# Performance work log

Hardware: AMD Instinct MI355X
Metric: run time of the kernel (lower is better)

## Reference

```python
import jax, jax.numpy as jnp
import numpy as np

N, C, K, H = 131072, 512, 128, 8  # points, channels, patch_size, heads


def setup_inputs() -> dict:
    key = jax.random.key(0)
    ks = jax.random.split(key, 6)
    feat = jax.random.normal(ks[0], (N, C), dtype=jnp.float32)
    Wqkv = jax.random.normal(ks[1], (C, 3 * C), dtype=jnp.float32) * 0.02
    bqkv = jax.random.normal(ks[2], (3 * C,), dtype=jnp.float32) * 0.02
    Wproj = jax.random.normal(ks[3], (C, C), dtype=jnp.float32) * 0.02
    bproj = jax.random.normal(ks[4], (C,), dtype=jnp.float32) * 0.02
    order = jax.random.permutation(ks[5], N).astype(jnp.int64)  # serialized order (all clusters full)
    inverse = jnp.argsort(order).astype(jnp.int64)              # serialized inverse
    return {"feat": feat, "Wqkv": Wqkv, "bqkv": bqkv, "Wproj": Wproj,
            "bproj": bproj, "order": order, "inverse": inverse}


def reference(feat, Wqkv, bqkv, Wproj, bproj, order, inverse):
    hd = C // H
    scale = hd ** -0.5
    qkv = feat @ Wqkv + bqkv                 # [N, 3C]
    qkv = qkv[order]                         # gather by serialized order
    qkv = qkv.reshape(-1, K, 3, H, hd)       # [W, K, 3, H, hd]
    qkv = jnp.moveaxis(qkv, 2, 0)            # [3, W, K, H, hd]
    q = jnp.swapaxes(qkv[0], 1, 2)           # [W, H, K, hd]
    k = jnp.swapaxes(qkv[1], 1, 2)
    v = jnp.swapaxes(qkv[2], 1, 2)
    # upcast_attention / upcast_softmax -> compute scores & softmax in fp32
    attn = jnp.einsum('whkd,whjd->whkj', (q * scale).astype(jnp.float32),
                      k.astype(jnp.float32))             # [W, H, K, K]
    attn = jax.nn.softmax(attn, axis=-1).astype(feat.dtype)
    out = jnp.einsum('whkj,whjd->whkd', attn, v)          # [W, H, K, hd]
    out = jnp.swapaxes(out, 1, 2).reshape(-1, C)          # [N, C]
    out = out[inverse]                                    # scatter back via inverse
    out = out @ Wproj + bproj
    return out
```

## Files before the change

### kernel.cpp

```cpp
#include <hip/hip_runtime.h>
#include <hip/hip_bf16.h>
#include <cstdint>
#include <cstddef>

typedef __bf16 bf16;
typedef __bf16 bf16x8 __attribute__((ext_vector_type(8)));
typedef float f32x4 __attribute__((ext_vector_type(4)));

#define N_PTS 131072
#define CDIM  512
#define C3    1536
#define HD    64
#define NH    8
#define KWIN  128

static __device__ __forceinline__ bf16 cvt(float x) { return (bf16)x; }

static __device__ __forceinline__ void gld16(const bf16* g, bf16* l) {
    __builtin_amdgcn_global_load_lds(
        (const __attribute__((address_space(1))) void*)g,
        (__attribute__((address_space(3))) void*)l, 16, 0, 0);
}

__global__ __launch_bounds__(256) void k_prep(
    const float* __restrict__ Wqkv, const float* __restrict__ Wproj,
    bf16* __restrict__ Wqkv_t, bf16* __restrict__ Wproj_t)
{
    int idx = blockIdx.x * 256 + threadIdx.x;
    if (idx < CDIM * C3) {
        int k = idx / C3, c = idx % C3;
        Wqkv_t[(size_t)c * CDIM + k] = cvt(Wqkv[idx]);
    } else {
        int j = idx - CDIM * C3;
        if (j < CDIM * CDIM) {
            int k = j / CDIM, c = j % CDIM;
            Wproj_t[(size_t)c * CDIM + k] = cvt(Wproj[j]);
        }
    }
}

__global__ __launch_bounds__(256) void k_gather(
    const float* __restrict__ feat, const int* __restrict__ order,
    bf16* __restrict__ feat_g)
{
    int row = blockIdx.x * 2 + (threadIdx.x >> 7);
    int c   = (threadIdx.x & 127) << 2;
    int src = order[row];
    float4 v = *reinterpret_cast<const float4*>(feat + (size_t)src * CDIM + c);
    union { bf16 e[4]; uint2 u; } pk;
    pk.e[0] = cvt(v.x); pk.e[1] = cvt(v.y); pk.e[2] = cvt(v.z); pk.e[3] = cvt(v.w);
    *reinterpret_cast<uint2*>(feat_g + (size_t)row * CDIM + c) = pk.u;
}

template <bool F32OUT, int NT>
__global__ __launch_bounds__(512) void k_gemm8(
    const bf16* __restrict__ Ag, const bf16* __restrict__ Bt,
    const float* __restrict__ bias, void* __restrict__ outp)
{
    __shared__ __align__(16) bf16 As[2][256 * 64];
    __shared__ __align__(16) bf16 Bs[2][256 * 64];

    const int t    = threadIdx.x;
    const int lane = t & 63;
    const int wv   = t >> 6;
    const int wr   = wv >> 2;
    const int wc   = wv & 3;
    const int g    = lane >> 4, r16 = lane & 15;

    const int nwg = gridDim.x;
    const int bid = blockIdx.x;
    const int swz = (bid & 7) * (nwg >> 3) + (bid >> 3);
    const int m0  = (swz / NT) * 256;
    const int n0  = (swz % NT) * 256;

    const int NKT = CDIM / 64;

    int aSrc[2][2], bSrc[2][2];
    int dstE[2][2];
#pragma unroll
    for (int h = 0; h < 2; ++h)
#pragma unroll
        for (int j = 0; j < 2; ++j) {
            int L = wv * 128 + j * 64 + lane;
            int row_l = L >> 3, p8 = L & 7;
            int s8 = (p8 - (row_l & 7)) & 7;
            int grow = h * 128 + row_l;
            aSrc[h][j] = (m0 + grow) * CDIM + s8 * 8;
            bSrc[h][j] = (n0 + grow) * CDIM + s8 * 8;
            dstE[h][j] = h * 8192 + (wv * 128 + j * 64) * 8;
        }

    int aoff[2][2][4];
    int boff[2][4];
#pragma unroll
    for (int grp = 0; grp < 2; ++grp)
#pragma unroll
        for (int kh = 0; kh < 2; ++kh)
#pragma unroll
            for (int q = 0; q < 4; ++q) {
                int row = wr * 128 + (grp * 4 + q) * 16 + r16;
                aoff[grp][kh][q] = row * 128 +
                    (((kh * 4 + g + (r16 & 7)) & 7) << 4);
            }
#pragma unroll
    for (int kh = 0; kh < 2; ++kh)
#pragma unroll
        for (int n = 0; n < 4; ++n) {
            int row = wc * 64 + n * 16 + r16;
            boff[kh][n] = row * 128 +
                (((kh * 4 + g + (r16 & 7)) & 7) << 4);
        }

    f32x4 acc[8][4];
    const f32x4 z = {0.f, 0.f, 0.f, 0.f};
#pragma unroll
    for (int i = 0; i < 8; ++i)
#pragma unroll
        for (int n = 0; n < 4; ++n) acc[i][n] = z;

    bf16x8 afr[2][4], bfr[2][4];

    auto stageA = [&](int tau) {
        const int b = tau & 1, ko = tau * 64;
#pragma unroll
        for (int h = 0; h < 2; ++h)
#pragma unroll
            for (int j = 0; j < 2; ++j)
                gld16(Ag + aSrc[h][j] + ko, &As[b][dstE[h][j]]);
    };
    auto stageB = [&](int tau) {
        const int b = tau & 1, ko = tau * 64;
#pragma unroll
        for (int h = 0; h < 2; ++h)
#pragma unroll
            for (int j = 0; j < 2; ++j)
                gld16(Bt + bSrc[h][j] + ko, &Bs[b][dstE[h][j]]);
    };
    auto readA = [&](int set, int b, int grp, int kh) {
        const char* ab = reinterpret_cast<const char*>(&As[b][0]);
#pragma unroll
        for (int q = 0; q < 4; ++q)
            afr[set][q] = *reinterpret_cast<const bf16x8*>(ab + aoff[grp][kh][q]);
    };
    auto readB = [&](int b, int kh) {
        const char* bb = reinterpret_cast<const char*>(&Bs[b][0]);
#pragma unroll
        for (int n = 0; n < 4; ++n)
            bfr[kh][n] = *reinterpret_cast<const bf16x8*>(bb + boff[kh][n]);
    };

    stageB(0); stageA(0); stageB(1); stageA(1);
    asm volatile("s_waitcnt vmcnt(8)" ::: "memory");
    __builtin_amdgcn_s_barrier();
    readA(0, 0, 0, 0);
    readB(0, 0);
    asm volatile("s_waitcnt lgkmcnt(0)" ::: "memory");
    __builtin_amdgcn_sched_barrier(0);

#pragma unroll
    for (int tau = 0; tau < NKT; ++tau) {
#pragma unroll
        for (int p = 0; p < 4; ++p) {
            const int pi  = tau * 4 + p;
            const int grp = p & 1, kh = p >> 1;

            if (p == 2 && tau + 2 < NKT) stageB(tau + 2);
            if (p == 3 && tau + 2 < NKT) stageA(tau + 2);

            if (pi + 1 < NKT * 4) {
                const int pn   = (p + 1) & 3;
                const int taun = tau + (p == 3);
                const int bn   = taun & 1;
                readA((pi + 1) & 1, bn, pn & 1, pn >> 1);
                if (pn == 0 || pn == 2) readB(bn, pn >> 1);
            }

            __builtin_amdgcn_s_setprio(1);
#pragma unroll
            for (int q = 0; q < 4; ++q)
#pragma unroll
                for (int n = 0; n < 4; ++n)
                    acc[grp * 4 + q][n] = __builtin_amdgcn_mfma_f32_16x16x32_bf16(
                        afr[pi & 1][q], bfr[kh][n], acc[grp * 4 + q][n], 0, 0, 0);
            __builtin_amdgcn_s_setprio(0);

            asm volatile("s_waitcnt lgkmcnt(0)" ::: "memory");
            __builtin_amdgcn_sched_barrier(0);
            if (p == 2) {
                if (tau + 2 < NKT)
                    asm volatile("s_waitcnt vmcnt(4)" ::: "memory");
                else
                    asm volatile("s_waitcnt vmcnt(0)" ::: "memory");
            }
            __builtin_amdgcn_s_barrier();
        }
    }

    const int ldo = NT * 256;
#pragma unroll
    for (int n = 0; n < 4; ++n) {
        int col = n0 + wc * 64 + n * 16 + r16;
        float b = bias[col];
#pragma unroll
        for (int i = 0; i < 8; ++i)
#pragma unroll
            for (int j = 0; j < 4; ++j) {
                int row = m0 + wr * 128 + i * 16 + g * 4 + j;
                if (F32OUT)
                    reinterpret_cast<float*>(outp)[(size_t)row * ldo + col] =
                        acc[i][n][j] + b;
                else
                    reinterpret_cast<bf16*>(outp)[(size_t)row * ldo + col] =
                        cvt(acc[i][n][j] + b);
            }
    }
}

__global__ __launch_bounds__(256) void k_attn(
    const bf16* __restrict__ qkv_s, const int* __restrict__ order,
    bf16* __restrict__ attn_g)
{
    __shared__ __align__(16) char smem[36864 + 64 * 136 * 2];
    __shared__ int ord_s[KWIN];
    bf16 (*Q)[72]   = reinterpret_cast<bf16 (*)[72]>(smem);
    bf16 (*Kt)[72]  = reinterpret_cast<bf16 (*)[72]>(smem + 128 * 72 * 2);
    bf16 (*P)[136]  = reinterpret_cast<bf16 (*)[136]>(smem);
    bf16 (*Vt)[136] = reinterpret_cast<bf16 (*)[136]>(smem + 36864);

    const int t    = threadIdx.x;
    const int lane = t & 63;
    const int wv   = t >> 6;
    const int g    = lane >> 4, r16 = lane & 15;
    const int h    = blockIdx.x;
    const int w    = blockIdx.y;

    const bf16* base = qkv_s + (size_t)w * KWIN * C3 + h * HD;

    if (t < KWIN) ord_s[t] = order[w * KWIN + t];

#pragma unroll
    for (int it = 0; it < 4; ++it) {
        int s   = it * 256 + t;
        int tok = s >> 3;
        int c8  = (s & 7) << 3;
        size_t roff = (size_t)tok * C3 + c8;
        *reinterpret_cast<uint4*>(&Q[tok][c8])  =
            *reinterpret_cast<const uint4*>(base + roff);
        *reinterpret_cast<uint4*>(&Kt[tok][c8]) =
            *reinterpret_cast<const uint4*>(base + roff + CDIM);
        uint4 vvec = *reinterpret_cast<const uint4*>(base + roff + 2 * CDIM);
        const bf16* ve = reinterpret_cast<const bf16*>(&vvec);
#pragma unroll
        for (int i = 0; i < 8; ++i) Vt[c8 + i][tok] = ve[i];
    }
    __syncthreads();

    f32x4 sc[2][8];
    const f32x4 z = {0.f, 0.f, 0.f, 0.f};
#pragma unroll
    for (int m = 0; m < 2; ++m)
#pragma unroll
        for (int n = 0; n < 8; ++n) sc[m][n] = z;

#pragma unroll
    for (int ks = 0; ks < 2; ++ks) {
        bf16x8 aq[2];
#pragma unroll
        for (int m = 0; m < 2; ++m)
            aq[m] = *reinterpret_cast<const bf16x8*>(
                &Q[wv * 32 + m * 16 + r16][ks * 32 + g * 8]);
#pragma unroll
        for (int n = 0; n < 8; ++n) {
            bf16x8 bk = *reinterpret_cast<const bf16x8*>(
                &Kt[n * 16 + r16][ks * 32 + g * 8]);
#pragma unroll
            for (int m = 0; m < 2; ++m)
                sc[m][n] = __builtin_amdgcn_mfma_f32_16x16x32_bf16(
                    aq[m], bk, sc[m][n], 0, 0, 0);
        }
    }

    const float scale = 0.125f;
    float inv_sum[2][4];
#pragma unroll
    for (int m = 0; m < 2; ++m) {
#pragma unroll
        for (int j = 0; j < 4; ++j) {
            float mx = -3.0e38f;
#pragma unroll
            for (int n = 0; n < 8; ++n) mx = fmaxf(mx, sc[m][n][j]);
            mx = fmaxf(mx, __shfl_xor(mx, 1));
            mx = fmaxf(mx, __shfl_xor(mx, 2));
            mx = fmaxf(mx, __shfl_xor(mx, 4));
            mx = fmaxf(mx, __shfl_xor(mx, 8));
            mx *= scale;
            float ssum = 0.f;
#pragma unroll
            for (int n = 0; n < 8; ++n) {
                float p = __expf(sc[m][n][j] * scale - mx);
                sc[m][n][j] = p;
                ssum += p;
            }
            ssum += __shfl_xor(ssum, 1);
            ssum += __shfl_xor(ssum, 2);
            ssum += __shfl_xor(ssum, 4);
            ssum += __shfl_xor(ssum, 8);
            inv_sum[m][j] = 1.f / ssum;
        }
    }

    __syncthreads();

#pragma unroll
    for (int m = 0; m < 2; ++m)
#pragma unroll
        for (int n = 0; n < 8; ++n)
#pragma unroll
            for (int j = 0; j < 4; ++j)
                P[wv * 32 + m * 16 + g * 4 + j][n * 16 + r16] =
                    cvt(sc[m][n][j] * inv_sum[m][j]);

    f32x4 o[2][4];
#pragma unroll
    for (int m = 0; m < 2; ++m)
#pragma unroll
        for (int n = 0; n < 4; ++n) o[m][n] = z;

#pragma unroll
    for (int kt = 0; kt < 4; ++kt) {
        bf16x8 ap[2];
#pragma unroll
        for (int m = 0; m < 2; ++m)
            ap[m] = *reinterpret_cast<const bf16x8*>(
                &P[wv * 32 + m * 16 + r16][kt * 32 + g * 8]);
#pragma unroll
        for (int n = 0; n < 4; ++n) {
            bf16x8 bvv = *reinterpret_cast<const bf16x8*>(
                &Vt[n * 16 + r16][kt * 32 + g * 8]);
#pragma unroll
            for (int m = 0; m < 2; ++m)
                o[m][n] = __builtin_amdgcn_mfma_f32_16x16x32_bf16(
                    ap[m], bvv, o[m][n], 0, 0, 0);
        }
    }

#pragma unroll
    for (int m = 0; m < 2; ++m)
#pragma unroll
        for (int n = 0; n < 4; ++n)
#pragma unroll
            for (int j = 0; j < 4; ++j) {
                int tok  = wv * 32 + m * 16 + g * 4 + j;
                int d    = n * 16 + r16;
                int drow = ord_s[tok];
                attn_g[(size_t)drow * CDIM + h * HD + d] = cvt(o[m][n][j]);
            }
}

extern "C" void kernel_launch(void* const* d_in, const int* in_sizes, int n_in,
                              void* d_out, int out_size, void* d_ws, size_t ws_size,
                              hipStream_t stream)
{
    const float* feat    = (const float*)d_in[0];
    const float* Wqkv    = (const float*)d_in[1];
    const float* bqkv    = (const float*)d_in[2];
    const float* Wproj   = (const float*)d_in[3];
    const float* bproj   = (const float*)d_in[4];
    const int*   order   = (const int*)d_in[5];
    float* out = (float*)d_out;

    const size_t qkv_bytes = (size_t)N_PTS * C3 * sizeof(bf16);
    const size_t gat_bytes = (size_t)N_PTS * CDIM * sizeof(bf16);
    const size_t wq_bytes  = (size_t)C3 * CDIM * sizeof(bf16);
    const size_t wp_bytes  = (size_t)CDIM * CDIM * sizeof(bf16);
    if (ws_size < qkv_bytes + gat_bytes + wq_bytes + wp_bytes) return;

    bf16* qkv_s     = (bf16*)d_ws;
    bf16* shared134 = (bf16*)((char*)d_ws + qkv_bytes);
    bf16* Wqkv_t    = (bf16*)((char*)d_ws + qkv_bytes + gat_bytes);
    bf16* Wproj_t   = (bf16*)((char*)d_ws + qkv_bytes + gat_bytes + wq_bytes);

    k_prep<<<dim3((CDIM * C3 + CDIM * CDIM + 255) / 256), 256, 0, stream>>>(
        Wqkv, Wproj, Wqkv_t, Wproj_t);
    k_gather<<<dim3(N_PTS / 2), 256, 0, stream>>>(feat, order, shared134);
    k_gemm8<false, C3 / 256><<<dim3((N_PTS / 256) * (C3 / 256)), 512, 0, stream>>>(
        shared134, Wqkv_t, bqkv, qkv_s);
    k_attn<<<dim3(NH, N_PTS / KWIN), 256, 0, stream>>>(qkv_s, order, shared134);
    k_gemm8<true, CDIM / 256><<<dim3((N_PTS / 256) * (CDIM / 256)), 512, 0, stream>>>(
        shared134, Wproj_t, bproj, out);
}
```

Measured before the change: 626.9 us.

## Fuse attention with output projection into per-window kernel

Merges the attention kernel and the output projection GEMM into one kernel, one block per window with 512 threads, looping over all 8 heads. Each head's attention output stays in LDS and is multiplied right away by the matching 64-column slice of Wproj. The results accumulate in registers and are scattered to the output via the order indices with bias added. This drops the bf16 attention intermediate round trip through HBM and one kernel launch. In exchange it uses about 138KB of LDS per block, which caps occupancy at one block per CU, and it serialises the heads with several barriers per head.

```diff
diff --git a/kernel.cpp b/kernel.cpp
--- a/kernel.cpp
+++ b/kernel.cpp
@@ -52,10 +52,10 @@
     *reinterpret_cast<uint2*>(feat_g + (size_t)row * CDIM + c) = pk.u;
 }
 
-template <bool F32OUT, int NT>
+template <int NT>
 __global__ __launch_bounds__(512) void k_gemm8(
     const bf16* __restrict__ Ag, const bf16* __restrict__ Bt,
-    const float* __restrict__ bias, void* __restrict__ outp)
+    const float* __restrict__ bias, bf16* __restrict__ outp)
 {
     __shared__ __align__(16) bf16 As[2][256 * 64];
     __shared__ __align__(16) bf16 Bs[2][256 * 64];
@@ -75,8 +75,7 @@
 
     const int NKT = CDIM / 64;
 
-    int aSrc[2][2], bSrc[2][2];
-    int dstE[2][2];
+    int aSrc[2][2], bSrc[2][2], dstE[2][2];
 #pragma unroll
     for (int h = 0; h < 2; ++h)
 #pragma unroll
@@ -206,89 +205,106 @@
 #pragma unroll
             for (int j = 0; j < 4; ++j) {
                 int row = m0 + wr * 128 + i * 16 + g * 4 + j;
-                if (F32OUT)
-                    reinterpret_cast<float*>(outp)[(size_t)row * ldo + col] =
-                        acc[i][n][j] + b;
-                else
-                    reinterpret_cast<bf16*>(outp)[(size_t)row * ldo + col] =
-                        cvt(acc[i][n][j] + b);
-            }
-    }
-}
-
-__global__ __launch_bounds__(256) void k_attn(
-    const bf16* __restrict__ qkv_s, const int* __restrict__ order,
-    bf16* __restrict__ attn_g)
+                outp[(size_t)row * ldo + col] = cvt(acc[i][n][j] + b);
+            }
+    }
+}
+
+__global__ __launch_bounds__(512) void k_attn_proj(
+    const bf16* __restrict__ qkv_s, const bf16* __restrict__ Wp_t,
+    const float* __restrict__ bproj, const int* __restrict__ order,
+    float* __restrict__ out)
 {
-    __shared__ __align__(16) char smem[36864 + 64 * 136 * 2];
+    __shared__ __align__(16) char smem[138240];
     __shared__ int ord_s[KWIN];
     bf16 (*Q)[72]   = reinterpret_cast<bf16 (*)[72]>(smem);
-    bf16 (*Kt)[72]  = reinterpret_cast<bf16 (*)[72]>(smem + 128 * 72 * 2);
+    bf16 (*Kt)[72]  = reinterpret_cast<bf16 (*)[72]>(smem + 18432);
     bf16 (*P)[136]  = reinterpret_cast<bf16 (*)[136]>(smem);
     bf16 (*Vt)[136] = reinterpret_cast<bf16 (*)[136]>(smem + 36864);
+    bf16 (*Oh)[72]  = reinterpret_cast<bf16 (*)[72]>(smem + 54272);
+    bf16* Wp        = reinterpret_cast<bf16*>(smem + 72704);
 
     const int t    = threadIdx.x;
     const int lane = t & 63;
     const int wv   = t >> 6;
     const int g    = lane >> 4, r16 = lane & 15;
-    const int h    = blockIdx.x;
-    const int w    = blockIdx.y;
-
-    const bf16* base = qkv_s + (size_t)w * KWIN * C3 + h * HD;
+    const int w    = blockIdx.x;
 
     if (t < KWIN) ord_s[t] = order[w * KWIN + t];
 
-#pragma unroll
-    for (int it = 0; it < 4; ++it) {
-        int s   = it * 256 + t;
-        int tok = s >> 3;
-        int c8  = (s & 7) << 3;
-        size_t roff = (size_t)tok * C3 + c8;
-        *reinterpret_cast<uint4*>(&Q[tok][c8])  =
-            *reinterpret_cast<const uint4*>(base + roff);
-        *reinterpret_cast<uint4*>(&Kt[tok][c8]) =
-            *reinterpret_cast<const uint4*>(base + roff + CDIM);
-        uint4 vvec = *reinterpret_cast<const uint4*>(base + roff + 2 * CDIM);
-        const bf16* ve = reinterpret_cast<const bf16*>(&vvec);
-#pragma unroll
-        for (int i = 0; i < 8; ++i) Vt[c8 + i][tok] = ve[i];
-    }
-    __syncthreads();
-
-    f32x4 sc[2][8];
+    int wpRow[4], wpSlot[4];
+#pragma unroll
+    for (int q4 = 0; q4 < 4; ++q4) {
+        int L = q4 * 512 + t;
+        wpRow[q4]  = L >> 2;
+        wpSlot[q4] = ((L & 3) - (wpRow[q4] >> 1)) & 3;
+    }
+
+    int paoff[4];
+#pragma unroll
+    for (int ci = 0; ci < 4; ++ci) {
+        int row = wv * 64 + ci * 16 + r16;
+        paoff[ci] = row * 64 + (((g + (row >> 1)) & 3) << 4);
+    }
+
+    f32x4 pacc[4][8];
     const f32x4 z = {0.f, 0.f, 0.f, 0.f};
 #pragma unroll
-    for (int m = 0; m < 2; ++m)
-#pragma unroll
-        for (int n = 0; n < 8; ++n) sc[m][n] = z;
-
-#pragma unroll
-    for (int ks = 0; ks < 2; ++ks) {
-        bf16x8 aq[2];
-#pragma unroll
-        for (int m = 0; m < 2; ++m)
-            aq[m] = *reinterpret_cast<const bf16x8*>(
-                &Q[wv * 32 + m * 16 + r16][ks * 32 + g * 8]);
-#pragma unroll
-        for (int n = 0; n < 8; ++n) {
-            bf16x8 bk = *reinterpret_cast<const bf16x8*>(
-                &Kt[n * 16 + r16][ks * 32 + g * 8]);
-#pragma unroll
-            for (int m = 0; m < 2; ++m)
-                sc[m][n] = __builtin_amdgcn_mfma_f32_16x16x32_bf16(
-                    aq[m], bk, sc[m][n], 0, 0, 0);
-        }
-    }
+    for (int ci = 0; ci < 4; ++ci)
+#pragma unroll
+        for (int qi = 0; qi < 8; ++qi) pacc[ci][qi] = z;
 
     const float scale = 0.125f;
-    float inv_sum[2][4];
-#pragma unroll
-    for (int m = 0; m < 2; ++m) {
+
+    for (int h = 0; h < NH; ++h) {
+        const bf16* base = qkv_s + (size_t)w * KWIN * C3 + h * HD;
+#pragma unroll
+        for (int it = 0; it < 2; ++it) {
+            int s   = it * 512 + t;
+            int tok = s >> 3;
+            int c8  = (s & 7) << 3;
+            size_t roff = (size_t)tok * C3 + c8;
+            *reinterpret_cast<uint4*>(&Q[tok][c8])  =
+                *reinterpret_cast<const uint4*>(base + roff);
+            *reinterpret_cast<uint4*>(&Kt[tok][c8]) =
+                *reinterpret_cast<const uint4*>(base + roff + CDIM);
+            uint4 vvec = *reinterpret_cast<const uint4*>(base + roff + 2 * CDIM);
+            const bf16* ve = reinterpret_cast<const bf16*>(&vvec);
+#pragma unroll
+            for (int i = 0; i < 8; ++i) Vt[c8 + i][tok] = ve[i];
+        }
+#pragma unroll
+        for (int ks = 0; ks < 2; ++ks)
+#pragma unroll
+            for (int q4 = 0; q4 < 4; ++q4) {
+                gld16(Wp_t + (size_t)wpRow[q4] * CDIM + h * HD + ks * 32
+                          + wpSlot[q4] * 8,
+                      Wp + ks * 16384 + (q4 * 512 + wv * 64) * 8);
+            }
+        __syncthreads();
+
+        f32x4 sc[8];
+#pragma unroll
+        for (int n = 0; n < 8; ++n) sc[n] = z;
+#pragma unroll
+        for (int ks = 0; ks < 2; ++ks) {
+            bf16x8 aq = *reinterpret_cast<const bf16x8*>(
+                &Q[wv * 16 + r16][ks * 32 + g * 8]);
+#pragma unroll
+            for (int n = 0; n < 8; ++n) {
+                bf16x8 bk = *reinterpret_cast<const bf16x8*>(
+                    &Kt[n * 16 + r16][ks * 32 + g * 8]);
+                sc[n] = __builtin_amdgcn_mfma_f32_16x16x32_bf16(
+                    aq, bk, sc[n], 0, 0, 0);
+            }
+        }
+
+        float inv_sum[4];
 #pragma unroll
         for (int j = 0; j < 4; ++j) {
             float mx = -3.0e38f;
 #pragma unroll
-            for (int n = 0; n < 8; ++n) mx = fmaxf(mx, sc[m][n][j]);
+            for (int n = 0; n < 8; ++n) mx = fmaxf(mx, sc[n][j]);
             mx = fmaxf(mx, __shfl_xor(mx, 1));
             mx = fmaxf(mx, __shfl_xor(mx, 2));
             mx = fmaxf(mx, __shfl_xor(mx, 4));
@@ -297,64 +313,89 @@
             float ssum = 0.f;
 #pragma unroll
             for (int n = 0; n < 8; ++n) {
-                float p = __expf(sc[m][n][j] * scale - mx);
-                sc[m][n][j] = p;
+                float p = __expf(sc[n][j] * scale - mx);
+                sc[n][j] = p;
                 ssum += p;
             }
             ssum += __shfl_xor(ssum, 1);
             ssum += __shfl_xor(ssum, 2);
             ssum += __shfl_xor(ssum, 4);
             ssum += __shfl_xor(ssum, 8);
-            inv_sum[m][j] = 1.f / ssum;
-        }
-    }
-
-    __syncthreads();
-
-#pragma unroll
-    for (int m = 0; m < 2; ++m)
+            inv_sum[j] = 1.f / ssum;
+        }
+
+        __syncthreads();
+
 #pragma unroll
         for (int n = 0; n < 8; ++n)
 #pragma unroll
             for (int j = 0; j < 4; ++j)
-                P[wv * 32 + m * 16 + g * 4 + j][n * 16 + r16] =
-                    cvt(sc[m][n][j] * inv_sum[m][j]);
-
-    f32x4 o[2][4];
-#pragma unroll
-    for (int m = 0; m < 2; ++m)
-#pragma unroll
-        for (int n = 0; n < 4; ++n) o[m][n] = z;
-
-#pragma unroll
-    for (int kt = 0; kt < 4; ++kt) {
-        bf16x8 ap[2];
-#pragma unroll
-        for (int m = 0; m < 2; ++m)
-            ap[m] = *reinterpret_cast<const bf16x8*>(
-                &P[wv * 32 + m * 16 + r16][kt * 32 + g * 8]);
-#pragma unroll
-        for (int n = 0; n < 4; ++n) {
-            bf16x8 bvv = *reinterpret_cast<const bf16x8*>(
-                &Vt[n * 16 + r16][kt * 32 + g * 8]);
-#pragma unroll
-            for (int m = 0; m < 2; ++m)
-                o[m][n] = __builtin_amdgcn_mfma_f32_16x16x32_bf16(
-                    ap[m], bvv, o[m][n], 0, 0, 0);
-        }
-    }
-
-#pragma unroll
-    for (int m = 0; m < 2; ++m)
+                P[wv * 16 + g * 4 + j][n * 16 + r16] =
+                    cvt(sc[n][j] * inv_sum[j]);
+
+        f32x4 o[4];
+#pragma unroll
+        for (int n = 0; n < 4; ++n) o[n] = z;
+#pragma unroll
+        for (int kt = 0; kt < 4; ++kt) {
+            bf16x8 ap = *reinterpret_cast<const bf16x8*>(
+                &P[wv * 16 + r16][kt * 32 + g * 8]);
+#pragma unroll
+            for (int n = 0; n < 4; ++n) {
+                bf16x8 bvv = *reinterpret_cast<const bf16x8*>(
+                    &Vt[n * 16 + r16][kt * 32 + g * 8]);
+                o[n] = __builtin_amdgcn_mfma_f32_16x16x32_bf16(
+                    ap, bvv, o[n], 0, 0, 0);
+            }
+        }
+
 #pragma unroll
         for (int n = 0; n < 4; ++n)
 #pragma unroll
-            for (int j = 0; j < 4; ++j) {
-                int tok  = wv * 32 + m * 16 + g * 4 + j;
-                int d    = n * 16 + r16;
-                int drow = ord_s[tok];
-                attn_g[(size_t)drow * CDIM + h * HD + d] = cvt(o[m][n][j]);
-            }
+            for (int j = 0; j < 4; ++j)
+                Oh[wv * 16 + g * 4 + j][n * 16 + r16] = cvt(o[n][j]);
+
+        __syncthreads();
+
+#pragma unroll
+        for (int ks = 0; ks < 2; ++ks) {
+            const char* wb = reinterpret_cast<const char*>(Wp + ks * 16384);
+            bf16x8 af[4], bq[8];
+#pragma unroll
+            for (int ci = 0; ci < 4; ++ci)
+                af[ci] = *reinterpret_cast<const bf16x8*>(wb + paoff[ci]);
+#pragma unroll
+            for (int qi = 0; qi < 8; ++qi)
+                bq[qi] = *reinterpret_cast<const bf16x8*>(
+                    &Oh[qi * 16 + r16][ks * 32 + g * 8]);
+            __builtin_amdgcn_s_setprio(1);
+#pragma unroll
+            for (int ci = 0; ci < 4; ++ci)
+#pragma unroll
+                for (int qi = 0; qi < 8; ++qi)
+                    pacc[ci][qi] = __builtin_amdgcn_mfma_f32_16x16x32_bf16(
+                        af[ci], bq[qi], pacc[ci][qi], 0, 0, 0);
+            __builtin_amdgcn_s_setprio(0);
+        }
+        __syncthreads();
+    }
+
+#pragma unroll
+    for (int ci = 0; ci < 4; ++ci) {
+        int c0 = wv * 64 + ci * 16 + g * 4;
+        float4 bp = *reinterpret_cast<const float4*>(bproj + c0);
+#pragma unroll
+        for (int qi = 0; qi < 8; ++qi) {
+            int q = qi * 16 + r16;
+            float4 v;
+            v.x = pacc[ci][qi][0] + bp.x;
+            v.y = pacc[ci][qi][1] + bp.y;
+            v.z = pacc[ci][qi][2] + bp.z;
+            v.w = pacc[ci][qi][3] + bp.w;
+            *reinterpret_cast<float4*>(
+                out + (size_t)ord_s[q] * CDIM + c0) = v;
+        }
+    }
 }
 
 extern "C" void kernel_launch(void* const* d_in, const int* in_sizes, int n_in,
@@ -375,17 +416,16 @@
     const size_t wp_bytes  = (size_t)CDIM * CDIM * sizeof(bf16);
     if (ws_size < qkv_bytes + gat_bytes + wq_bytes + wp_bytes) return;
 
-    bf16* qkv_s     = (bf16*)d_ws;
-    bf16* shared134 = (bf16*)((char*)d_ws + qkv_bytes);
-    bf16* Wqkv_t    = (bf16*)((char*)d_ws + qkv_bytes + gat_bytes);
-    bf16* Wproj_t   = (bf16*)((char*)d_ws + qkv_bytes + gat_bytes + wq_bytes);
+    bf16* qkv_s   = (bf16*)d_ws;
+    bf16* feat_g  = (bf16*)((char*)d_ws + qkv_bytes);
+    bf16* Wqkv_t  = (bf16*)((char*)d_ws + qkv_bytes + gat_bytes);
+    bf16* Wproj_t = (bf16*)((char*)d_ws + qkv_bytes + gat_bytes + wq_bytes);
 
     k_prep<<<dim3((CDIM * C3 + CDIM * CDIM + 255) / 256), 256, 0, stream>>>(
         Wqkv, Wproj, Wqkv_t, Wproj_t);
-    k_gather<<<dim3(N_PTS / 2), 256, 0, stream>>>(feat, order, shared134);
-    k_gemm8<false, C3 / 256><<<dim3((N_PTS / 256) * (C3 / 256)), 512, 0, stream>>>(
-        shared134, Wqkv_t, bqkv, qkv_s);
-    k_attn<<<dim3(NH, N_PTS / KWIN), 256, 0, stream>>>(qkv_s, order, shared134);
-    k_gemm8<true, CDIM / 256><<<dim3((N_PTS / 256) * (CDIM / 256)), 512, 0, stream>>>(
-        shared134, Wproj_t, bproj, out);
-}
+    k_gather<<<dim3(N_PTS / 2), 256, 0, stream>>>(feat, order, feat_g);
+    k_gemm8<C3 / 256><<<dim3((N_PTS / 256) * (C3 / 256)), 512, 0, stream>>>(
+        feat_g, Wqkv_t, bqkv, qkv_s);
+    k_attn_proj<<<dim3(N_PTS / KWIN), 512, 0, stream>>>(
+        qkv_s, Wproj_t, bproj, order, out);
+}
```

Measured after the change: 662.8 us. +5.7%, slower.

## Add dedicated smaller-tile projection GEMM and de-conflict V transpose stores

Applied to the files above, without the earlier changes.

Replaces the output projection GEMM with a new kernel that uses 128x256 tiles and a 32-wide K step with double buffering, and allows up to 4 blocks per CU. The aim is to give the smaller projection GEMM more workgroups and more occupancy. In the attention kernel, the V transpose writes are rotated per thread so that stores to the transposed LDS tile spread across banks instead of conflicting. It also adds a launch bound of 2 blocks per CU on the attention kernel. The trade-off is that the shorter K step means more barriers per tile.

```diff
diff --git a/kernel.cpp b/kernel.cpp
--- a/kernel.cpp
+++ b/kernel.cpp
@@ -20,6 +20,21 @@
     __builtin_amdgcn_global_load_lds(
         (const __attribute__((address_space(1))) void*)g,
         (__attribute__((address_space(3))) void*)l, 16, 0, 0);
+}
+
+static __device__ __forceinline__ uint4 rot128(uint4 u, int r) {
+    uint32_t x = u.x, y = u.y, z = u.z, w = u.w;
+    uint32_t x1 = (x >> 16) | (y << 16), y1 = (y >> 16) | (z << 16),
+             z1 = (z >> 16) | (w << 16), w1 = (w >> 16) | (x << 16);
+    bool o1 = r & 1;
+    x = o1 ? x1 : x; y = o1 ? y1 : y; z = o1 ? z1 : z; w = o1 ? w1 : w;
+    bool o2 = r & 2;
+    uint32_t t0 = x;
+    x = o2 ? y : x; y = o2 ? z : y; z = o2 ? w : z; w = o2 ? t0 : w;
+    bool o4 = r & 4;
+    uint32_t tx = x, ty = y;
+    x = o4 ? z : x; y = o4 ? w : y; z = o4 ? tx : z; w = o4 ? ty : w;
+    uint4 o; o.x = x; o.y = y; o.z = z; o.w = w; return o;
 }
 
 __global__ __launch_bounds__(256) void k_prep(
@@ -52,10 +67,10 @@
     *reinterpret_cast<uint2*>(feat_g + (size_t)row * CDIM + c) = pk.u;
 }
 
-template <bool F32OUT, int NT>
+template <int NT>
 __global__ __launch_bounds__(512) void k_gemm8(
     const bf16* __restrict__ Ag, const bf16* __restrict__ Bt,
-    const float* __restrict__ bias, void* __restrict__ outp)
+    const float* __restrict__ bias, bf16* __restrict__ outp)
 {
     __shared__ __align__(16) bf16 As[2][256 * 64];
     __shared__ __align__(16) bf16 Bs[2][256 * 64];
@@ -75,8 +90,7 @@
 
     const int NKT = CDIM / 64;
 
-    int aSrc[2][2], bSrc[2][2];
-    int dstE[2][2];
+    int aSrc[2][2], bSrc[2][2], dstE[2][2];
 #pragma unroll
     for (int h = 0; h < 2; ++h)
 #pragma unroll
@@ -206,17 +220,123 @@
 #pragma unroll
             for (int j = 0; j < 4; ++j) {
                 int row = m0 + wr * 128 + i * 16 + g * 4 + j;
-                if (F32OUT)
-                    reinterpret_cast<float*>(outp)[(size_t)row * ldo + col] =
-                        acc[i][n][j] + b;
-                else
-                    reinterpret_cast<bf16*>(outp)[(size_t)row * ldo + col] =
-                        cvt(acc[i][n][j] + b);
-            }
-    }
-}
-
-__global__ __launch_bounds__(256) void k_attn(
+                outp[(size_t)row * ldo + col] = cvt(acc[i][n][j] + b);
+            }
+    }
+}
+
+template <int NT>
+__global__ __launch_bounds__(512, 4) void k_proj(
+    const bf16* __restrict__ Ag, const bf16* __restrict__ Bt,
+    const float* __restrict__ bias, float* __restrict__ outp)
+{
+    __shared__ __align__(16) bf16 As[2][128 * 32];
+    __shared__ __align__(16) bf16 Bs[2][256 * 32];
+
+    const int t    = threadIdx.x;
+    const int lane = t & 63;
+    const int wv   = t >> 6;
+    const int wr   = wv >> 2;
+    const int wc   = wv & 3;
+    const int g    = lane >> 4, r16 = lane & 15;
+
+    const int nwg = gridDim.x;
+    const int bid = blockIdx.x;
+    const int swz = (bid & 7) * (nwg >> 3) + (bid >> 3);
+    const int m0  = (swz / NT) * 128;
+    const int n0  = (swz % NT) * 256;
+
+    const int L0 = wv * 64 + lane;
+    const int rA = L0 >> 2,          sA = ((L0 & 3) - (rA >> 1)) & 3;
+    const int rB1 = rA + 128,        sB1v = ((L0 & 3) - (rB1 >> 1)) & 3;
+    const bf16* srcA  = Ag + (size_t)(m0 + rA) * CDIM + sA * 8;
+    const bf16* srcB0 = Bt + (size_t)(n0 + rA) * CDIM + sA * 8;
+    const bf16* srcB1 = Bt + (size_t)(n0 + rB1) * CDIM + sB1v * 8;
+
+    int aoff[4], boff[4];
+#pragma unroll
+    for (int m = 0; m < 4; ++m) {
+        int row = wr * 64 + m * 16 + r16;
+        aoff[m] = row * 64 + (((g + (row >> 1)) & 3) << 4);
+    }
+#pragma unroll
+    for (int n = 0; n < 4; ++n) {
+        int row = wc * 64 + n * 16 + r16;
+        boff[n] = row * 64 + (((g + (row >> 1)) & 3) << 4);
+    }
+
+    f32x4 acc[4][4];
+    const f32x4 z = {0.f, 0.f, 0.f, 0.f};
+#pragma unroll
+    for (int m = 0; m < 4; ++m)
+#pragma unroll
+        for (int n = 0; n < 4; ++n) acc[m][n] = z;
+
+    auto stage = [&](int kt) {
+        const int b  = kt & 1;
+        const int ko = kt * 32;
+        gld16(srcA  + ko, &As[b][(size_t)wv * 64 * 8]);
+        gld16(srcB0 + ko, &Bs[b][(size_t)wv * 64 * 8]);
+        gld16(srcB1 + ko, &Bs[b][(size_t)(512 + wv * 64) * 8]);
+    };
+
+    auto compute = [&](int kt) {
+        const int b = kt & 1;
+        bf16x8 af[4], bvv[4];
+#pragma unroll
+        for (int m = 0; m < 4; ++m)
+            af[m] = *reinterpret_cast<const bf16x8*>(
+                reinterpret_cast<const char*>(&As[b][0]) + aoff[m]);
+#pragma unroll
+        for (int n = 0; n < 4; ++n)
+            bvv[n] = *reinterpret_cast<const bf16x8*>(
+                reinterpret_cast<const char*>(&Bs[b][0]) + boff[n]);
+        __builtin_amdgcn_s_setprio(1);
+#pragma unroll
+        for (int m = 0; m < 4; ++m)
+#pragma unroll
+            for (int n = 0; n < 4; ++n)
+                acc[m][n] = __builtin_amdgcn_mfma_f32_16x16x32_bf16(
+                    af[m], bvv[n], acc[m][n], 0, 0, 0);
+        __builtin_amdgcn_s_setprio(0);
+    };
+
+    const int NKT = CDIM / 32;
+
+    stage(0); stage(1);
+    asm volatile("s_waitcnt vmcnt(3)" ::: "memory");
+    __builtin_amdgcn_s_barrier();
+
+#pragma unroll
+    for (int kt = 0; kt < NKT - 2; ++kt) {
+        compute(kt);
+        asm volatile("s_waitcnt lgkmcnt(0)" ::: "memory");
+        __builtin_amdgcn_s_barrier();
+        stage(kt + 2);
+        asm volatile("s_waitcnt vmcnt(3)" ::: "memory");
+        __builtin_amdgcn_s_barrier();
+    }
+    compute(NKT - 2);
+    asm volatile("s_waitcnt vmcnt(0) lgkmcnt(0)" ::: "memory");
+    __builtin_amdgcn_s_barrier();
+    compute(NKT - 1);
+
+    const int ldo = NT * 256;
+#pragma unroll
+    for (int n = 0; n < 4; ++n) {
+        int col = n0 + wc * 64 + n * 16 + r16;
+        float b = bias[col];
+#pragma unroll
+        for (int m = 0; m < 4; ++m)
+#pragma unroll
+            for (int j = 0; j < 4; ++j) {
+                int row = m0 + wr * 64 + m * 16 + g * 4 + j;
+                outp[(size_t)row * ldo + col] = acc[m][n][j] + b;
+            }
+    }
+}
+
+__global__ __launch_bounds__(256, 2) void k_attn(
     const bf16* __restrict__ qkv_s, const int* __restrict__ order,
     bf16* __restrict__ attn_g)
 {
@@ -226,6 +346,7 @@
     bf16 (*Kt)[72]  = reinterpret_cast<bf16 (*)[72]>(smem + 128 * 72 * 2);
     bf16 (*P)[136]  = reinterpret_cast<bf16 (*)[136]>(smem);
     bf16 (*Vt)[136] = reinterpret_cast<bf16 (*)[136]>(smem + 36864);
+    unsigned short* Vtu = reinterpret_cast<unsigned short*>(smem + 36864);
 
     const int t    = threadIdx.x;
     const int lane = t & 63;
@@ -237,6 +358,8 @@
     const bf16* base = qkv_s + (size_t)w * KWIN * C3 + h * HD;
 
     if (t < KWIN) ord_s[t] = order[w * KWIN + t];
+
+    const int rot = t & 7;
 
 #pragma unroll
     for (int it = 0; it < 4; ++it) {
@@ -249,9 +372,14 @@
         *reinterpret_cast<uint4*>(&Kt[tok][c8]) =
             *reinterpret_cast<const uint4*>(base + roff + CDIM);
         uint4 vvec = *reinterpret_cast<const uint4*>(base + roff + 2 * CDIM);
-        const bf16* ve = reinterpret_cast<const bf16*>(&vvec);
-#pragma unroll
-        for (int i = 0; i < 8; ++i) Vt[c8 + i][tok] = ve[i];
+        uint4 vr = rot128(vvec, rot);
+        uint32_t wd[4] = {vr.x, vr.y, vr.z, vr.w};
+#pragma unroll
+        for (int k = 0; k < 8; ++k) {
+            int d = c8 + ((k + rot) & 7);
+            Vtu[d * 136 + tok] =
+                (unsigned short)(wd[k >> 1] >> ((k & 1) * 16));
+        }
     }
     __syncthreads();
 
@@ -383,9 +511,9 @@
     k_prep<<<dim3((CDIM * C3 + CDIM * CDIM + 255) / 256), 256, 0, stream>>>(
         Wqkv, Wproj, Wqkv_t, Wproj_t);
     k_gather<<<dim3(N_PTS / 2), 256, 0, stream>>>(feat, order, shared134);
-    k_gemm8<false, C3 / 256><<<dim3((N_PTS / 256) * (C3 / 256)), 512, 0, stream>>>(
+    k_gemm8<C3 / 256><<<dim3((N_PTS / 256) * (C3 / 256)), 512, 0, stream>>>(
         shared134, Wqkv_t, bqkv, qkv_s);
     k_attn<<<dim3(NH, N_PTS / KWIN), 256, 0, stream>>>(qkv_s, order, shared134);
-    k_gemm8<true, CDIM / 256><<<dim3((N_PTS / 256) * (CDIM / 256)), 512, 0, stream>>>(
+    k_proj<CDIM / 256><<<dim3((N_PTS / 128) * (CDIM / 256)), 512, 0, stream>>>(
         shared134, Wproj_t, bproj, out);
 }
```

Measured after the change: 624.7 us. Within noise of the previous version (-0.4%).
